# Performance work log

Hardware: AMD Instinct MI355X
Metric: run time of the kernel (lower is better)

The kernel has to match this reference:

```python
import jax, jax.numpy as jnp
import numpy as np

N = 4096        # batch size (rows)
K = 4           # instances per class -> num_instances in the torch code
D = 256         # embedding dim
MARGIN = 0.5
SAMPLE_KEY = jax.random.key(42)  # fixed key: deterministic stand-in for torch.multinomial


def setup_inputs() -> dict:
    key = jax.random.key(0)
    x = jax.random.normal(key, (N, D), dtype=jnp.float32)
    # L2-normalize like typical metric-learning embeddings so sims are in [-1, 1]
    inputs = x / jnp.linalg.norm(x, axis=1, keepdims=True)
    targets = (jnp.arange(N) // K).astype(jnp.int32)  # P*K batch: equal-size classes
    return {"inputs": inputs, "targets": targets}


def reference(inputs, targets):
    n = inputs.shape[0]
    km1 = K - 1                 # positives per row
    n_neg = n - K               # negatives per row

    sim = inputs @ inputs.T                                   # [n, n]
    same = targets[:, None] == targets[None, :]
    eye = jnp.eye(n, dtype=bool)
    pos_mask = same & ~eye
    neg_mask = ~same

    # masked_select + per-row sort: masked entries -> +inf, ascending sort,
    # keep first count entries (counts are uniform across rows)
    pos_sorted = jnp.sort(jnp.where(pos_mask, sim, jnp.inf), axis=1)[:, :km1]   # [n, K-1]
    neg_sorted = jnp.sort(jnp.where(neg_mask, sim, jnp.inf), axis=1)[:, :n_neg] # [n, n-K]

    pos_d = jnp.mean(pos_sorted)
    neg_d = jnp.mean(neg_sorted)

    # GaussDistribution per row over negatives
    neg_mean = jnp.mean(neg_sorted, axis=1, keepdims=True)
    neg_std = jnp.sqrt(jnp.mean((neg_sorted - neg_mean) ** 2, axis=1, keepdims=True))
    # NOTE: the original uses exp(+(x-mu)^2 / (2 sigma^2)) (no minus sign) -- faithful
    logprob = (neg_sorted - neg_mean) ** 2 / (2.0 * neg_std ** 2)               # [n, n-K]

    # multinomial without replacement ~ Gumbel top-k on log-weights
    gumbel = -jnp.log(-jnp.log(
        jax.random.uniform(SAMPLE_KEY, logprob.shape, minval=1e-20, maxval=1.0)))
    _, neg_idx = jax.lax.top_k(logprob + gumbel, km1)                            # [n, K-1]
    neg_pair = jnp.take_along_axis(neg_sorted, neg_idx, axis=1)                  # [n, K-1]

    pos_loss = jnp.mean(jnp.log1p(jnp.exp(-2.0 * (pos_sorted - MARGIN))), axis=1)
    neg_loss = 0.04 * jnp.mean(jnp.log1p(jnp.exp(50.0 * (neg_pair - MARGIN))), axis=1)
    loss = jnp.sum(pos_loss + neg_loss) / n

    # prec: fraction of rows where hardest positive > hardest sampled negative + 0.05
    c = jnp.sum(pos_sorted[:, -1] > jnp.max(neg_pair, axis=1) + 0.05)
    prec = c.astype(jnp.float32) / n

    return loss, prec, pos_d, neg_d
```

## Files before the change

kernel.cpp:

```cpp
#include <hip/hip_runtime.h>
#include <hip/hip_bf16.h>
#include <cstdint>
#include <cfloat>
#include <math.h>

#define NN 4096
#define DD 256
#define KC 4
#define NNEG 4092
#define MARGIN 0.5f
#define NB 1024

__device__ __forceinline__ uint32_t rotl32(uint32_t x, int r) {
  return (x << r) | (x >> (32 - r));
}

__device__ __forceinline__ void threefry2x32_42(uint32_t x0, uint32_t x1,
                                                uint32_t& o0, uint32_t& o1) {
  const uint32_t k0 = 0u, k1 = 42u;
  const uint32_t k2 = k0 ^ k1 ^ 0x1BD11BDAu;
  x0 += k0; x1 += k1;
#define TF_R(r) { x0 += x1; x1 = rotl32(x1, r); x1 ^= x0; }
  TF_R(13) TF_R(15) TF_R(26) TF_R(6)
  x0 += k1; x1 += k2 + 1u;
  TF_R(17) TF_R(29) TF_R(16) TF_R(24)
  x0 += k2; x1 += k0 + 2u;
  TF_R(13) TF_R(15) TF_R(26) TF_R(6)
  x0 += k0; x1 += k1 + 3u;
  TF_R(17) TF_R(29) TF_R(16) TF_R(24)
  x0 += k1; x1 += k2 + 4u;
  TF_R(13) TF_R(15) TF_R(26) TF_R(6)
  x0 += k2; x1 += k0 + 5u;
#undef TF_R
  o0 = x0; o1 = x1;
}

__device__ __forceinline__ float gumbel_at(uint32_t f) {
  uint32_t o0, o1;
  threefry2x32_42(0u, f, o0, o1);
  uint32_t bits = o0 ^ o1;
  uint32_t fb = (bits >> 9) | 0x3F800000u;
  float fl = __uint_as_float(fb) - 1.0f;
  float u = fmaxf(1e-20f, fl + 1e-20f);
  return -logf(-logf(u));
}

#define TS 64
#define LDSS 68

__global__ __launch_bounds__(256) void gemm_sim(const float* __restrict__ X,
                                                float* __restrict__ S) {
  __shared__ float As[TS * LDSS];
  __shared__ float Bs[TS * LDSS];
  const int tid = threadIdx.x;
  const int tx = tid & 15, ty = tid >> 4;
  const int rowBase = blockIdx.y * TS, colBase = blockIdx.x * TS;
  float acc[4][4] = {};
  for (int kb = 0; kb < DD; kb += TS) {
#pragma unroll
    for (int it = 0; it < 4; ++it) {
      int idx = tid + 256 * it;
      int r = idx >> 4, c4 = idx & 15;
      float4 av = *(const float4*)(X + (size_t)(rowBase + r) * DD + kb + c4 * 4);
      float4 bv = *(const float4*)(X + (size_t)(colBase + r) * DD + kb + c4 * 4);
      *(float4*)(As + r * LDSS + c4 * 4) = av;
      *(float4*)(Bs + r * LDSS + c4 * 4) = bv;
    }
    __syncthreads();
    for (int k = 0; k < TS; k += 4) {
      float4 a[4], b[4];
#pragma unroll
      for (int i = 0; i < 4; ++i) a[i] = *(const float4*)(As + (ty + 16 * i) * LDSS + k);
#pragma unroll
      for (int j = 0; j < 4; ++j) b[j] = *(const float4*)(Bs + (tx + 16 * j) * LDSS + k);
#pragma unroll
      for (int i = 0; i < 4; ++i)
#pragma unroll
        for (int j = 0; j < 4; ++j) {
          acc[i][j] += a[i].x * b[j].x;
          acc[i][j] += a[i].y * b[j].y;
          acc[i][j] += a[i].z * b[j].z;
          acc[i][j] += a[i].w * b[j].w;
        }
    }
    __syncthreads();
  }
#pragma unroll
  for (int i = 0; i < 4; ++i)
#pragma unroll
    for (int j = 0; j < 4; ++j)
      S[(size_t)(rowBase + ty + 16 * i) * NN + colBase + tx + 16 * j] = acc[i][j];
}

__global__ __launch_bounds__(256) void row_kernel(const float* __restrict__ S,
                                                  float* __restrict__ acc) {
  __shared__ uint32_t hist[NB];
  __shared__ uint32_t offs[NB];
  __shared__ float sval[NN];
  __shared__ float sh[24];
  __shared__ uint32_t wtot[4];

  const int row = blockIdx.x;
  const int tid = threadIdx.x;
  const int lane = tid & 63, wid = tid >> 6;

#pragma unroll
  for (int i = 0; i < NB / 256; ++i) hist[tid + 256 * i] = 0;

  const float4* src = (const float4*)(S + (size_t)row * NN);
  const int pslot = row >> 2;
  float vv[16];
#pragma unroll
  for (int it = 0; it < 4; ++it) {
    int slot = tid + 256 * it;
    float4 t4 = src[slot];
    if (slot == pslot) {
      sh[16] = t4.x; sh[17] = t4.y; sh[18] = t4.z; sh[19] = t4.w;
      t4.x = INFINITY; t4.y = INFINITY; t4.z = INFINITY; t4.w = INFINITY;
    }
    vv[4 * it + 0] = t4.x; vv[4 * it + 1] = t4.y;
    vv[4 * it + 2] = t4.z; vv[4 * it + 3] = t4.w;
  }
  __syncthreads();

#pragma unroll
  for (int e = 0; e < 16; ++e) {
    float t = fminf(fmaxf((vv[e] + 0.5f) * (float)NB, 0.0f), (float)(NB - 1));
    atomicAdd(&hist[(int)t], 1u);
  }
  __syncthreads();

  uint32_t h[4];
  uint32_t s4 = 0;
#pragma unroll
  for (int j = 0; j < 4; ++j) { h[j] = hist[tid * 4 + j]; s4 += h[j]; }
  uint32_t inc = s4;
#pragma unroll
  for (int off = 1; off < 64; off <<= 1) {
    uint32_t n = __shfl_up(inc, (unsigned)off, 64);
    if (lane >= off) inc += n;
  }
  if (lane == 63) wtot[wid] = inc;

  if (tid == 0) {
    int self = row & 3;
    float p[3]; int m = 0;
#pragma unroll
    for (int c = 0; c < 4; ++c)
      if (c != self) p[m++] = sh[16 + c];
    float t;
    if (p[0] > p[1]) { t = p[0]; p[0] = p[1]; p[1] = t; }
    if (p[1] > p[2]) { t = p[1]; p[1] = p[2]; p[2] = t; }
    if (p[0] > p[1]) { t = p[0]; p[0] = p[1]; p[1] = t; }
    sh[0] = p[0]; sh[1] = p[1]; sh[2] = p[2];
  }
  __syncthreads();
  uint32_t wbase = 0;
  for (int w = 0; w < wid; ++w) wbase += wtot[w];
  uint32_t run = wbase + inc - s4;
#pragma unroll
  for (int j = 0; j < 4; ++j) { offs[tid * 4 + j] = run; run += h[j]; }
  __syncthreads();

  int slt[16];
#pragma unroll
  for (int e = 0; e < 16; ++e) {
    float v = vv[e];
    float t = fminf(fmaxf((v + 0.5f) * (float)NB, 0.0f), (float)(NB - 1));
    int b = (int)t;
    uint32_t s = atomicAdd(&offs[b], 1u);
    sval[s] = v;
    slt[e] = (int)s;
  }
  __syncthreads();

#pragma unroll
  for (int e = 0; e < 16; ++e) {
    float v = vv[e];
    float t = fminf(fmaxf((v + 0.5f) * (float)NB, 0.0f), (float)(NB - 1));
    int b = (int)t;
    uint32_t end = offs[b];
    uint32_t st = end - hist[b];
    int s = slt[e];
    int cnt = (int)st;
    for (uint32_t u = st; u < end; ++u) {
      float w = sval[u];
      if (w < v || (w == v && (int)u < s)) cnt++;
    }
    slt[e] = cnt;
  }

  float s = 0.0f;
#pragma unroll
  for (int e = 0; e < 16; ++e) if (vv[e] < 1e30f) s += vv[e];
#pragma unroll
  for (int off = 32; off > 0; off >>= 1) s += __shfl_down(s, off, 64);
  if (lane == 0) sh[5 + wid] = s;
  __syncthreads();
  if (tid == 0) {
    float tot = sh[5] + sh[6] + sh[7] + sh[8];
    sh[9] = tot;
    sh[3] = tot / (float)NNEG;
  }
  __syncthreads();
  const float mu = sh[3];

  float q = 0.0f;
#pragma unroll
  for (int e = 0; e < 16; ++e)
    if (vv[e] < 1e30f) { float d = vv[e] - mu; q += d * d; }
#pragma unroll
  for (int off = 32; off > 0; off >>= 1) q += __shfl_down(q, off, 64);
  if (lane == 0) sh[10 + wid] = q;
  __syncthreads();
  if (tid == 0) {
    float var = (sh[10] + sh[11] + sh[12] + sh[13]) / (float)NNEG;
    float sd = sqrtf(var);
    sh[4] = 1.0f / (2.0f * sd * sd);
  }
  __syncthreads();
  const float inv2s2 = sh[4];

  float* rs = sval;
  float* rv = sval + 768;
  float s0 = -FLT_MAX, s1 = -FLT_MAX, s2 = -FLT_MAX;
  float v0 = 0.0f, v1 = 0.0f, v2 = 0.0f;
  const uint32_t fbase = (uint32_t)row * (uint32_t)NNEG;
#pragma unroll
  for (int e = 0; e < 16; ++e) {
    float v = vv[e];
    if (v < 1e30f) {
      float d = v - mu;
      float sc = d * d * inv2s2 + gumbel_at(fbase + (uint32_t)slt[e]);
      if (sc > s2) {
        if (sc > s1) {
          s2 = s1; v2 = v1;
          if (sc > s0) { s1 = s0; v1 = v0; s0 = sc; v0 = v; }
          else         { s1 = sc; v1 = v; }
        } else { s2 = sc; v2 = v; }
      }
    }
  }
  rs[tid * 3 + 0] = s0; rv[tid * 3 + 0] = v0;
  rs[tid * 3 + 1] = s1; rv[tid * 3 + 1] = v1;
  rs[tid * 3 + 2] = s2; rv[tid * 3 + 2] = v2;
  __syncthreads();

  if (tid < 64) {
    float g0 = -FLT_MAX, g1 = -FLT_MAX, g2 = -FLT_MAX;
    float w0 = 0.0f, w1 = 0.0f, w2 = 0.0f;
    for (int blk = 0; blk < 4; ++blk) {
      int b0 = (tid + 64 * blk) * 3;
      for (int e = 0; e < 3; ++e) {
        float sc = rs[b0 + e], v = rv[b0 + e];
        if (sc > g2) {
          if (sc > g1) {
            g2 = g1; w2 = w1;
            if (sc > g0) { g1 = g0; w1 = w0; g0 = sc; w0 = v; }
            else         { g1 = sc; w1 = v; }
          } else { g2 = sc; w2 = v; }
        }
      }
    }
    rs[tid * 3 + 0] = g0; rv[tid * 3 + 0] = w0;
    rs[tid * 3 + 1] = g1; rv[tid * 3 + 1] = w1;
    rs[tid * 3 + 2] = g2; rv[tid * 3 + 2] = w2;
  }
  __syncthreads();

  if (tid == 0) {
    float g0 = -FLT_MAX, g1 = -FLT_MAX, g2 = -FLT_MAX;
    float w0 = 0.0f, w1 = 0.0f, w2 = 0.0f;
    for (int i = 0; i < 192; ++i) {
      float sc = rs[i], v = rv[i];
      if (sc > g2) {
        if (sc > g1) {
          g2 = g1; w2 = w1;
          if (sc > g0) { g1 = g0; w1 = w0; g0 = sc; w0 = v; }
          else         { g1 = sc; w1 = v; }
        } else { g2 = sc; w2 = v; }
      }
    }
    float negmax = fmaxf(w0, fmaxf(w1, w2));
    float neg_loss = 0.04f * (log1pf(expf(50.0f * (w0 - MARGIN))) +
                              log1pf(expf(50.0f * (w1 - MARGIN))) +
                              log1pf(expf(50.0f * (w2 - MARGIN)))) / 3.0f;
    float p0 = sh[0], p1 = sh[1], p2 = sh[2];
    float pos_loss = (log1pf(expf(-2.0f * (p0 - MARGIN))) +
                      log1pf(expf(-2.0f * (p1 - MARGIN))) +
                      log1pf(expf(-2.0f * (p2 - MARGIN)))) / 3.0f;
    atomicAdd(&acc[0], pos_loss + neg_loss);
    if (p2 > negmax + 0.05f) atomicAdd(&acc[1], 1.0f);
    atomicAdd(&acc[2], p0 + p1 + p2);
    atomicAdd(&acc[3], sh[9]);
  }
}

__global__ void finalize(const float* __restrict__ acc, float* out) {
  if (threadIdx.x == 0 && blockIdx.x == 0) {
    out[0] = acc[0] / 4096.0f;
    out[1] = acc[1] / 4096.0f;
    out[2] = acc[2] / (4096.0f * 3.0f);
    out[3] = acc[3] / (4096.0f * 4092.0f);
  }
}

extern "C" void kernel_launch(void* const* d_in, const int* in_sizes, int n_in,
                              void* d_out, int out_size, void* d_ws, size_t ws_size,
                              hipStream_t stream) {
  (void)in_sizes; (void)n_in; (void)out_size; (void)ws_size;
  const float* X = (const float*)d_in[0];
  float* S = (float*)d_ws;
  float* acc = (float*)((char*)d_ws + (size_t)NN * NN * 4);
  hipMemsetAsync(acc, 0, 4 * sizeof(float), stream);
  dim3 grid(NN / TS, NN / TS);
  gemm_sim<<<grid, 256, 0, stream>>>(X, S);
  row_kernel<<<NN, 256, 0, stream>>>(S, acc);
  finalize<<<1, 64, 0, stream>>>(acc, (float*)d_out);
}
```

Baseline: 449.3 us.

## Use symmetric 128x128 GEMM tiles and finer histogram rank computation

```diff
diff --git a/kernel.cpp b/kernel.cpp
--- a/kernel.cpp
+++ b/kernel.cpp
@@ -6,10 +6,9 @@
 
 #define NN 4096
 #define DD 256
-#define KC 4
 #define NNEG 4092
 #define MARGIN 0.5f
-#define NB 1024
+#define NB 4096
 
 __device__ __forceinline__ uint32_t rotl32(uint32_t x, int r) {
   return (x << r) | (x >> (32 - r));
@@ -45,20 +44,31 @@
   return -logf(-logf(u));
 }
 
-#define TS 64
+__device__ __forceinline__ int bucket_of(float v) {
+  return (int)fminf(fmaxf((v + 0.5f) * (float)NB, 0.0f), (float)(NB - 1));
+}
+
+#define BT 128
+#define NT (NN / BT)
+#define BK 64
 #define LDSS 68
 
 __global__ __launch_bounds__(256) void gemm_sim(const float* __restrict__ X,
                                                 float* __restrict__ S) {
-  __shared__ float As[TS * LDSS];
-  __shared__ float Bs[TS * LDSS];
+  __shared__ float As[BT * LDSS];
+  __shared__ float Bs[BT * LDSS];
   const int tid = threadIdx.x;
   const int tx = tid & 15, ty = tid >> 4;
-  const int rowBase = blockIdx.y * TS, colBase = blockIdx.x * TS;
-  float acc[4][4] = {};
-  for (int kb = 0; kb < DD; kb += TS) {
-#pragma unroll
-    for (int it = 0; it < 4; ++it) {
+
+  int b = blockIdx.x, bi = 0;
+  while (b >= NT - bi) { b -= NT - bi; bi++; }
+  const int bj = bi + b;
+  const int rowBase = bi * BT, colBase = bj * BT;
+
+  float acc[8][8] = {};
+  for (int kb = 0; kb < DD; kb += BK) {
+#pragma unroll
+    for (int it = 0; it < 8; ++it) {
       int idx = tid + 256 * it;
       int r = idx >> 4, c4 = idx & 15;
       float4 av = *(const float4*)(X + (size_t)(rowBase + r) * DD + kb + c4 * 4);
@@ -67,29 +77,36 @@
       *(float4*)(Bs + r * LDSS + c4 * 4) = bv;
     }
     __syncthreads();
-    for (int k = 0; k < TS; k += 4) {
-      float4 a[4], b[4];
-#pragma unroll
-      for (int i = 0; i < 4; ++i) a[i] = *(const float4*)(As + (ty + 16 * i) * LDSS + k);
-#pragma unroll
-      for (int j = 0; j < 4; ++j) b[j] = *(const float4*)(Bs + (tx + 16 * j) * LDSS + k);
-#pragma unroll
-      for (int i = 0; i < 4; ++i)
-#pragma unroll
-        for (int j = 0; j < 4; ++j) {
-          acc[i][j] += a[i].x * b[j].x;
-          acc[i][j] += a[i].y * b[j].y;
-          acc[i][j] += a[i].z * b[j].z;
-          acc[i][j] += a[i].w * b[j].w;
+    for (int k = 0; k < BK; k += 4) {
+      float4 a[8], bfr[8];
+#pragma unroll
+      for (int i = 0; i < 8; ++i) a[i] = *(const float4*)(As + (ty + 16 * i) * LDSS + k);
+#pragma unroll
+      for (int j = 0; j < 8; ++j) bfr[j] = *(const float4*)(Bs + (tx + 16 * j) * LDSS + k);
+#pragma unroll
+      for (int i = 0; i < 8; ++i)
+#pragma unroll
+        for (int j = 0; j < 8; ++j) {
+          acc[i][j] += a[i].x * bfr[j].x;
+          acc[i][j] += a[i].y * bfr[j].y;
+          acc[i][j] += a[i].z * bfr[j].z;
+          acc[i][j] += a[i].w * bfr[j].w;
         }
     }
     __syncthreads();
   }
 #pragma unroll
-  for (int i = 0; i < 4; ++i)
-#pragma unroll
-    for (int j = 0; j < 4; ++j)
+  for (int i = 0; i < 8; ++i)
+#pragma unroll
+    for (int j = 0; j < 8; ++j)
       S[(size_t)(rowBase + ty + 16 * i) * NN + colBase + tx + 16 * j] = acc[i][j];
+  if (bi != bj) {
+#pragma unroll
+    for (int i = 0; i < 8; ++i)
+#pragma unroll
+      for (int j = 0; j < 8; ++j)
+        S[(size_t)(colBase + tx + 16 * j) * NN + rowBase + ty + 16 * i] = acc[i][j];
+  }
 }
 
 __global__ __launch_bounds__(256) void row_kernel(const float* __restrict__ S,
@@ -105,7 +122,8 @@
   const int lane = tid & 63, wid = tid >> 6;
 
 #pragma unroll
-  for (int i = 0; i < NB / 256; ++i) hist[tid + 256 * i] = 0;
+  for (int it = 0; it < 4; ++it)
+    ((uint4*)hist)[tid + 256 * it] = make_uint4(0u, 0u, 0u, 0u);
 
   const float4* src = (const float4*)(S + (size_t)row * NN);
   const int pslot = row >> 2;
@@ -121,26 +139,17 @@
     vv[4 * it + 0] = t4.x; vv[4 * it + 1] = t4.y;
     vv[4 * it + 2] = t4.z; vv[4 * it + 3] = t4.w;
   }
-  __syncthreads();
-
-#pragma unroll
-  for (int e = 0; e < 16; ++e) {
-    float t = fminf(fmaxf((vv[e] + 0.5f) * (float)NB, 0.0f), (float)(NB - 1));
-    atomicAdd(&hist[(int)t], 1u);
-  }
-  __syncthreads();
-
-  uint32_t h[4];
-  uint32_t s4 = 0;
-#pragma unroll
-  for (int j = 0; j < 4; ++j) { h[j] = hist[tid * 4 + j]; s4 += h[j]; }
-  uint32_t inc = s4;
-#pragma unroll
-  for (int off = 1; off < 64; off <<= 1) {
-    uint32_t n = __shfl_up(inc, (unsigned)off, 64);
-    if (lane >= off) inc += n;
-  }
-  if (lane == 63) wtot[wid] = inc;
+
+  float s = 0.0f;
+#pragma unroll
+  for (int e = 0; e < 16; ++e) if (vv[e] < 1e30f) s += vv[e];
+#pragma unroll
+  for (int off = 32; off > 0; off >>= 1) s += __shfl_down(s, off, 64);
+  if (lane == 0) sh[5 + wid] = s;
+  __syncthreads();
+
+#pragma unroll
+  for (int e = 0; e < 16; ++e) atomicAdd(&hist[bucket_of(vv[e])], 1u);
 
   if (tid == 0) {
     int self = row & 3;
@@ -153,58 +162,30 @@
     if (p[1] > p[2]) { t = p[1]; p[1] = p[2]; p[2] = t; }
     if (p[0] > p[1]) { t = p[0]; p[0] = p[1]; p[1] = t; }
     sh[0] = p[0]; sh[1] = p[1]; sh[2] = p[2];
-  }
-  __syncthreads();
-  uint32_t wbase = 0;
-  for (int w = 0; w < wid; ++w) wbase += wtot[w];
-  uint32_t run = wbase + inc - s4;
-#pragma unroll
-  for (int j = 0; j < 4; ++j) { offs[tid * 4 + j] = run; run += h[j]; }
-  __syncthreads();
-
-  int slt[16];
-#pragma unroll
-  for (int e = 0; e < 16; ++e) {
-    float v = vv[e];
-    float t = fminf(fmaxf((v + 0.5f) * (float)NB, 0.0f), (float)(NB - 1));
-    int b = (int)t;
-    uint32_t s = atomicAdd(&offs[b], 1u);
-    sval[s] = v;
-    slt[e] = (int)s;
-  }
-  __syncthreads();
-
-#pragma unroll
-  for (int e = 0; e < 16; ++e) {
-    float v = vv[e];
-    float t = fminf(fmaxf((v + 0.5f) * (float)NB, 0.0f), (float)(NB - 1));
-    int b = (int)t;
-    uint32_t end = offs[b];
-    uint32_t st = end - hist[b];
-    int s = slt[e];
-    int cnt = (int)st;
-    for (uint32_t u = st; u < end; ++u) {
-      float w = sval[u];
-      if (w < v || (w == v && (int)u < s)) cnt++;
-    }
-    slt[e] = cnt;
-  }
-
-  float s = 0.0f;
-#pragma unroll
-  for (int e = 0; e < 16; ++e) if (vv[e] < 1e30f) s += vv[e];
-#pragma unroll
-  for (int off = 32; off > 0; off >>= 1) s += __shfl_down(s, off, 64);
-  if (lane == 0) sh[5 + wid] = s;
-  __syncthreads();
-  if (tid == 0) {
     float tot = sh[5] + sh[6] + sh[7] + sh[8];
     sh[9] = tot;
     sh[3] = tot / (float)NNEG;
   }
   __syncthreads();
+
+  uint32_t h[16];
+  uint32_t s16 = 0;
+#pragma unroll
+  for (int jj = 0; jj < 4; ++jj) {
+    uint4 h4 = ((const uint4*)hist)[tid * 4 + jj];
+    h[4 * jj + 0] = h4.x; h[4 * jj + 1] = h4.y;
+    h[4 * jj + 2] = h4.z; h[4 * jj + 3] = h4.w;
+    s16 += h4.x + h4.y + h4.z + h4.w;
+  }
+  uint32_t inc = s16;
+#pragma unroll
+  for (int off = 1; off < 64; off <<= 1) {
+    uint32_t n = __shfl_up(inc, (unsigned)off, 64);
+    if (lane >= off) inc += n;
+  }
+  if (lane == 63) wtot[wid] = inc;
+
   const float mu = sh[3];
-
   float q = 0.0f;
 #pragma unroll
   for (int e = 0; e < 16; ++e)
@@ -213,25 +194,52 @@
   for (int off = 32; off > 0; off >>= 1) q += __shfl_down(q, off, 64);
   if (lane == 0) sh[10 + wid] = q;
   __syncthreads();
+
+  uint32_t wbase = 0;
+  for (int w = 0; w < wid; ++w) wbase += wtot[w];
+  uint32_t run = wbase + inc - s16;
+#pragma unroll
+  for (int jj = 0; jj < 4; ++jj) {
+    uint4 o4;
+    o4.x = run; run += h[4 * jj + 0];
+    o4.y = run; run += h[4 * jj + 1];
+    o4.z = run; run += h[4 * jj + 2];
+    o4.w = run; run += h[4 * jj + 3];
+    ((uint4*)offs)[tid * 4 + jj] = o4;
+  }
   if (tid == 0) {
     float var = (sh[10] + sh[11] + sh[12] + sh[13]) / (float)NNEG;
     float sd = sqrtf(var);
     sh[4] = 1.0f / (2.0f * sd * sd);
   }
   __syncthreads();
+
+#pragma unroll
+  for (int e = 0; e < 16; ++e) {
+    uint32_t sl = atomicAdd(&offs[bucket_of(vv[e])], 1u);
+    sval[sl] = vv[e];
+  }
+  __syncthreads();
+
   const float inv2s2 = sh[4];
-
-  float* rs = sval;
-  float* rv = sval + 768;
+  const uint32_t fbase = (uint32_t)row * (uint32_t)NNEG;
   float s0 = -FLT_MAX, s1 = -FLT_MAX, s2 = -FLT_MAX;
   float v0 = 0.0f, v1 = 0.0f, v2 = 0.0f;
-  const uint32_t fbase = (uint32_t)row * (uint32_t)NNEG;
-#pragma unroll
-  for (int e = 0; e < 16; ++e) {
-    float v = vv[e];
+#pragma unroll 1
+  for (int it = 0; it < 16; ++it) {
+    int sl = tid + 256 * it;
+    float v = sval[sl];
     if (v < 1e30f) {
+      int bk = bucket_of(v);
+      uint32_t end = offs[bk];
+      uint32_t st = end - hist[bk];
+      int cnt = (int)st;
+      for (uint32_t u = st; u < end; ++u) {
+        float w = sval[u];
+        cnt += (w < v || (w == v && (int)u < sl)) ? 1 : 0;
+      }
       float d = v - mu;
-      float sc = d * d * inv2s2 + gumbel_at(fbase + (uint32_t)slt[e]);
+      float sc = d * d * inv2s2 + gumbel_at(fbase + (uint32_t)cnt);
       if (sc > s2) {
         if (sc > s1) {
           s2 = s1; v2 = v1;
@@ -241,6 +249,10 @@
       }
     }
   }
+  __syncthreads();
+
+  float* rs = sval;
+  float* rv = sval + 768;
   rs[tid * 3 + 0] = s0; rv[tid * 3 + 0] = v0;
   rs[tid * 3 + 1] = s1; rv[tid * 3 + 1] = v1;
   rs[tid * 3 + 2] = s2; rv[tid * 3 + 2] = v2;
@@ -313,8 +325,7 @@
   float* S = (float*)d_ws;
   float* acc = (float*)((char*)d_ws + (size_t)NN * NN * 4);
   hipMemsetAsync(acc, 0, 4 * sizeof(float), stream);
-  dim3 grid(NN / TS, NN / TS);
-  gemm_sim<<<grid, 256, 0, stream>>>(X, S);
+  gemm_sim<<<NT * (NT + 1) / 2, 256, 0, stream>>>(X, S);
   row_kernel<<<NN, 256, 0, stream>>>(S, acc);
   finalize<<<1, 64, 0, stream>>>(acc, (float*)d_out);
 }
```

Measured after the change: 422.9 us. 1.06x faster.
